# Performance work log

Measured on AMD Instinct MI355X. Metric: run time of the kernel, lower is better.

Reference implementation:

```python
import jax, jax.numpy as jnp
import numpy as np
from jax import lax

N_LAYER = 24
N_EMBD = 1024
FFN = 4 * N_EMBD
LN_EPS = 1e-5


def setup_inputs() -> dict:
    key = jax.random.key(0)
    ks = jax.random.split(key, 24)
    L, C, F = N_LAYER, N_EMBD, FFN
    s = C ** -0.5  # keep GEMV outputs O(1) so exp() stays finite

    def rn(k, shape, scale=1.0):
        return jax.random.normal(k, shape, dtype=jnp.float32) * scale

    state = jnp.concatenate([
        rn(ks[1], (1, L, C)),                                          # statea: prev ln1 output
        rn(ks[2], (1, L, C), 0.1),                                     # stateb: wkv numerator acc
        jax.random.uniform(ks[3], (1, L, C), dtype=jnp.float32) + 0.5, # statec: wkv denominator acc (>0)
        rn(ks[4], (1, L, C)),                                          # stated: prev ln2 output
    ], axis=0)

    return {
        "x": rn(ks[0], (C,)),
        "state": state,
        "ln1w": 1.0 + rn(ks[5], (L, C), 0.02),
        "ln1b": rn(ks[6], (L, C), 0.02),
        "ln2w": 1.0 + rn(ks[7], (L, C), 0.02),
        "ln2b": rn(ks[8], (L, C), 0.02),
        "time_decay": -jnp.abs(rn(ks[9], (L, C))) - 0.1,
        "time_first": rn(ks[10], (L, C), 0.1),
        "kktk": jax.random.uniform(ks[11], (L, C), dtype=jnp.float32),
        "vvtv": jax.random.uniform(ks[12], (L, C), dtype=jnp.float32),
        "rrtr": jax.random.uniform(ks[13], (L, C), dtype=jnp.float32),
        "key": rn(ks[14], (L, 3, C, C), s),        # [kk, vv, -rr] stacks
        "outputv": rn(ks[15], (L, C, C), s),
        "time_mix_k_ffn": jax.random.uniform(ks[16], (L, C), dtype=jnp.float32),
        "time_mix_r_ffn": jax.random.uniform(ks[17], (L, C), dtype=jnp.float32),
        "key_ffn": rn(ks[18], (L, F, C), s),
        "receptance_ffn": rn(ks[19], (L, C, C), s),  # stored pre-negated, as in the module
        "value_ffn": rn(ks[20], (L, C, F), F ** -0.5),
    }


def _ln(v, w, b):
    m = v.mean()
    var = ((v - m) ** 2).mean()
    return (v - m) * lax.rsqrt(var + LN_EPS) * w + b


def reference(x, state, ln1w, ln1b, ln2w, ln2b, time_decay, time_first,
              kktk, vvtv, rrtr, key, outputv, time_mix_k_ffn, time_mix_r_ffn,
              key_ffn, receptance_ffn, value_ffn):
    # offset = 0, so the state slice covers all layers
    statea, stateb, statec, stated = state[0], state[1], state[2], state[3]  # each [L, C]
    # token-shift contributions precomputed against previous-step state
    kk_s = kktk * statea
    vv_s = vvtv * statea
    rr_s = rrtr * statea
    tmk_s = time_mix_k_ffn * stated
    tmr_s = time_mix_r_ffn * stated

    def layer(xc, p):
        (l1w, l1b, l2w, l2b, td, tfst, kks, vvs, rrs, keym, outv,
         tmk, tmr, kffn, rffn, vffn, sb, sc) = p
        xy = _ln(xc, l1w, l1b)
        k = keym[0] @ (xy + kks)
        v = keym[1] @ (xy + vvs)
        r = keym[2] @ (xy + rrs)   # keym[2] holds -receptance weights
        etfk = jnp.exp(tfst + k)
        w = (sb + etfk * v) / (sc * jnp.exp(r) + jnp.exp(tfst + k + r) + sc + etfk)
        sxx = xc + outv @ w
        ek = jnp.exp(k)
        ed = jnp.exp(td)
        sb_new = sb * ed + ek * v
        sc_new = sc * ed + ek
        xx = _ln(sxx, l2w, l2b)
        kf = jnp.square(jax.nn.relu(kffn @ (xx + tmk)))
        rf = jnp.exp(rffn @ (xx + tmr))  # rffn already negated
        x_new = sxx + (vffn @ kf) / (rf + 1.0)
        return x_new, (xy, sb_new, sc_new, xx)

    xs = (ln1w, ln1b, ln2w, ln2b, time_decay, time_first, kk_s, vv_s, rr_s,
          key, outputv, tmk_s, tmr_s, key_ffn, receptance_ffn, value_ffn,
          stateb, statec)
    x_out, (sa_n, sb_n, sc_n, sd_n) = lax.scan(layer, x, xs)
    new_state = jnp.stack([sa_n, sb_n, sc_n, sd_n])  # [4, L, C]
    return x_out, new_state
```

## Files before the change

kernel.cpp:

```cpp
#include <hip/hip_runtime.h>
#include <math.h>
#include <stddef.h>

#define NLAYER 24
#define NEMBD  1024
#define NFFN   4096
#define NB     256
#define NT     256
#define LN_EPS 1e-5f

#define OUT_SA (NEMBD)
#define OUT_SB (NEMBD + NLAYER*NEMBD)
#define OUT_SC (NEMBD + 2*NLAYER*NEMBD)
#define OUT_SD (NEMBD + 3*NLAYER*NEMBD)

typedef unsigned long long u64;
typedef unsigned u32;

#define QX_OFF    0
#define QW_OFF    1024
#define QSXX_OFF  2048
#define QKFB_OFF  3072
#define QTOTAL    7168

#define LMSK  0
#define LACT  3072
#define LFF   7168
#define LLN   27648
#define LXL   27656
#define LSXL  27660
#define LRFL  27664
#define LPT   27668
#define SMTOT 27684

struct Params {
  const float *x, *state, *ln1w, *ln1b, *ln2w, *ln2b, *td, *tf, *kktk, *vvtv, *rrtr;
  const float *key, *outputv, *tmk, *tmr, *kffn, *rffn, *vffn;
  float *out;
  u64 *q;
};

__device__ __forceinline__ float wred(float v) {
#pragma unroll
  for (int o = 32; o > 0; o >>= 1) v += __shfl_xor(v, o, 64);
  return v;
}
__device__ __forceinline__ float dot4(float4 a, float4 b) {
  return a.x*b.x + a.y*b.y + a.z*b.z + a.w*b.w;
}
__device__ __forceinline__ float fcomp(float4 v, int j) {
  return j == 0 ? v.x : (j == 1 ? v.y : (j == 2 ? v.z : v.w));
}
__device__ __forceinline__ u64 qload(const u64* a) {
  return __hip_atomic_load(a, __ATOMIC_RELAXED, __HIP_MEMORY_SCOPE_AGENT);
}
__device__ __forceinline__ void qput(u64* a, float v, u32 tag) {
  u64 w = ((u64)tag << 32) | (u64)__float_as_uint(v);
  __hip_atomic_store(a, w, __ATOMIC_RELAXED, __HIP_MEMORY_SCOPE_AGENT);
}
__device__ __forceinline__ u32   qtag(u64 w) { return (u32)(w >> 32); }
__device__ __forceinline__ float qval(u64 w) { return __uint_as_float((u32)w); }

__device__ __forceinline__ void stage16(const float* g, float* l) {
  __builtin_amdgcn_global_load_lds(
      (const __attribute__((address_space(1))) unsigned int*)g,
      (__attribute__((address_space(3))) unsigned int*)l, 16, 0, 0);
}

__device__ __forceinline__ void lbar() {
  asm volatile("s_waitcnt lgkmcnt(0)" ::: "memory");
  __builtin_amdgcn_s_barrier();
  asm volatile("" ::: "memory");
}

#define POLL4(QB, IDX, TG, OUTA)                                              \
  do {                                                                        \
    u64 a0_, a1_, a2_, a3_; long cc_ = 0;                                     \
    for (;;) {                                                                \
      a0_ = qload((QB) + (IDX) + 0); a1_ = qload((QB) + (IDX) + 1);           \
      a2_ = qload((QB) + (IDX) + 2); a3_ = qload((QB) + (IDX) + 3);           \
      if (qtag(a0_) >= (TG) && qtag(a1_) >= (TG) &&                           \
          qtag(a2_) >= (TG) && qtag(a3_) >= (TG)) break;                      \
      __builtin_amdgcn_s_sleep(1);                                            \
      if (++cc_ > (1L << 20)) break;            \
    }                                                                         \
    OUTA[0] = qval(a0_); OUTA[1] = qval(a1_);                                 \
    OUTA[2] = qval(a2_); OUTA[3] = qval(a3_);                                 \
  } while (0)

__global__ void __launch_bounds__(NT, 1)
rwkv_persistent(Params p) {
  const int b    = blockIdx.x;
  const int t    = threadIdx.x;
  const int wid  = t >> 6;
  const int lane = t & 63;
  const int i0   = t * 4;
  const int myi  = b * 4 + wid;

  __shared__ float sm[SMTOT];

  u64* QX   = p.q + QX_OFF;
  u64* QW   = p.q + QW_OFF;
  u64* QSXX = p.q + QSXX_OFF;
  u64* QKFB = p.q + QKFB_OFF;

  float4 wKEY[12];
  float4 wOV[4];
  float4 wVF[16];
  float4 pA[6];
  float4 pC[5];
  float s_tf, s_sb, s_sc, s_td;

  auto loadKEY = [&](int L) {
#pragma unroll
    for (int mth = 0; mth < 3; ++mth) {
      const float* W = p.key + ((size_t)L * 3 + mth) * NEMBD * NEMBD
                     + (size_t)myi * NEMBD + lane * 4;
#pragma unroll
      for (int c = 0; c < 4; ++c)
        wKEY[mth * 4 + c] = *(const float4*)&W[c * 256];
    }
  };
  auto loadOV = [&](int L) {
    const float* W = p.outputv + ((size_t)L * NEMBD + myi) * NEMBD + lane * 4;
#pragma unroll
    for (int c = 0; c < 4; ++c)
      wOV[c] = *(const float4*)&W[c * 256];
  };
  auto loadVF = [&](int L) {
#pragma unroll
    for (int r = 0; r < 4; ++r) {
      const float* W = p.vffn + ((size_t)L * NEMBD + b * 4 + r) * NFFN + lane * 4;
#pragma unroll
      for (int c = 0; c < 4; ++c)
        wVF[r * 4 + c] = *(const float4*)&W[(wid * 4 + c) * 256];
    }
  };
  auto stageFF = [&](int L) {
    float* slab = &sm[LFF + wid * 5120];
#pragma unroll
    for (int q = 0; q < 4; ++q) {
      const float* W = p.kffn + ((size_t)L * NFFN + b * 16 + wid * 4 + q) * NEMBD;
#pragma unroll
      for (int c = 0; c < 4; ++c)
        stage16(W + c * 256 + lane * 4, slab + q * 1024 + c * 256);
    }
    const float* Wr = p.rffn + ((size_t)L * NEMBD + myi) * NEMBD;
#pragma unroll
    for (int c = 0; c < 4; ++c)
      stage16(Wr + c * 256 + lane * 4, slab + 4096 + c * 256);
  };
  auto loadPA = [&](int L) {
    const int o = L * NEMBD + i0;
    pA[0] = *(const float4*)&p.ln1w[o];
    pA[1] = *(const float4*)&p.ln1b[o];
    pA[2] = *(const float4*)&p.state[0 * NLAYER * NEMBD + o];
    pA[3] = *(const float4*)&p.kktk[o];
    pA[4] = *(const float4*)&p.vvtv[o];
    pA[5] = *(const float4*)&p.rrtr[o];
    if (lane == 0) {
      const int ix = L * NEMBD + myi;
      s_tf = p.tf[ix];
      s_sb = p.state[1 * NLAYER * NEMBD + ix];
      s_sc = p.state[2 * NLAYER * NEMBD + ix];
      s_td = p.td[ix];
    }
  };
  auto loadPC = [&](int L) {
    const int o = L * NEMBD + i0;
    pC[0] = *(const float4*)&p.ln2w[o];
    pC[1] = *(const float4*)&p.ln2b[o];
    pC[2] = *(const float4*)&p.state[3 * NLAYER * NEMBD + o];
    pC[3] = *(const float4*)&p.tmk[o];
    pC[4] = *(const float4*)&p.tmr[o];
  };

  loadPA(0); loadKEY(0); loadOV(0);

  for (int l = 0; l < NLAYER; ++l) {
    const u32 t1 = (u32)(4 * l + 1), t2 = t1 + 1, t3 = t1 + 2, t4 = t1 + 3;

    {
      float xa[4];
      if (l == 0) {
        float4 x4 = *(const float4*)&p.x[i0];
        xa[0] = x4.x; xa[1] = x4.y; xa[2] = x4.z; xa[3] = x4.w;
      } else {
        POLL4(QX, i0, (u32)(4 * l), xa);
      }
      if (t == b) {
#pragma unroll
        for (int j = 0; j < 4; ++j) sm[LXL + j] = xa[j];
      }
      float s = xa[0] + xa[1] + xa[2] + xa[3];
      float q = xa[0]*xa[0] + xa[1]*xa[1] + xa[2]*xa[2] + xa[3]*xa[3];
      s = wred(s); q = wred(q);
      if (lane == 0) { sm[LLN + wid] = s; sm[LLN + 4 + wid] = q; }
      lbar();
      float m  = (sm[LLN+0] + sm[LLN+1] + sm[LLN+2] + sm[LLN+3]) * (1.f / NEMBD);
      float tq = (sm[LLN+4] + sm[LLN+5] + sm[LLN+6] + sm[LLN+7]) * (1.f / NEMBD);
      float rs = rsqrtf(tq - m * m + LN_EPS);
#pragma unroll
      for (int j = 0; j < 4; ++j) {
        int i = i0 + j;
        float xy  = (xa[j] - m) * rs * fcomp(pA[0], j) + fcomp(pA[1], j);
        float sav = fcomp(pA[2], j);
        sm[LMSK + i]        = xy + fcomp(pA[3], j) * sav;
        sm[LMSK + 1024 + i] = xy + fcomp(pA[4], j) * sav;
        sm[LMSK + 2048 + i] = xy + fcomp(pA[5], j) * sav;
        if (t == b) p.out[OUT_SA + l * NEMBD + i] = xy;
      }
      lbar();
      float a0 = 0.f, a1 = 0.f, a2 = 0.f;
#pragma unroll
      for (int c = 0; c < 4; ++c) {
        int col = lane * 4 + c * 256;
        a0 += dot4(wKEY[c],     *(const float4*)&sm[LMSK + col]);
        a1 += dot4(wKEY[4 + c], *(const float4*)&sm[LMSK + 1024 + col]);
        a2 += dot4(wKEY[8 + c], *(const float4*)&sm[LMSK + 2048 + col]);
      }
      a0 = wred(a0); a1 = wred(a1); a2 = wred(a2);
      if (lane == 0) {
        float etfk = expf(s_tf + a0);
        float er   = expf(a2);
        float wv = (s_sb + etfk * a1) / ((s_sc + etfk) * (1.f + er));
        qput(&QW[myi], wv, t1);
        float ek = expf(a0), ed = expf(s_td);
        p.out[OUT_SB + l * NEMBD + myi] = s_sb * ed + ek * a1;
        p.out[OUT_SC + l * NEMBD + myi] = s_sc * ed + ek;
      }
      stageFF(l); loadPC(l);
      lbar();
    }

    {
      float wv[4];
      POLL4(QW, i0, t1, wv);
#pragma unroll
      for (int j = 0; j < 4; ++j) sm[LMSK + i0 + j] = wv[j];
      lbar();
      float acc = 0.f;
#pragma unroll
      for (int c = 0; c < 4; ++c)
        acc += dot4(wOV[c], *(const float4*)&sm[LMSK + lane * 4 + c * 256]);
      acc = wred(acc);
      if (lane == 0) {
        float sxx = sm[LXL + wid] + acc;
        qput(&QSXX[myi], sxx, t2);
        sm[LSXL + wid] = sxx;
      }
      loadVF(l);
      lbar();
    }

    {
      float xa[4];
      POLL4(QSXX, i0, t2, xa);
      float s = xa[0] + xa[1] + xa[2] + xa[3];
      float q = xa[0]*xa[0] + xa[1]*xa[1] + xa[2]*xa[2] + xa[3]*xa[3];
      s = wred(s); q = wred(q);
      if (lane == 0) { sm[LLN + wid] = s; sm[LLN + 4 + wid] = q; }
      lbar();
      float m  = (sm[LLN+0] + sm[LLN+1] + sm[LLN+2] + sm[LLN+3]) * (1.f / NEMBD);
      float tq = (sm[LLN+4] + sm[LLN+5] + sm[LLN+6] + sm[LLN+7]) * (1.f / NEMBD);
      float rs = rsqrtf(tq - m * m + LN_EPS);
#pragma unroll
      for (int j = 0; j < 4; ++j) {
        int i = i0 + j;
        float xx  = (xa[j] - m) * rs * fcomp(pC[0], j) + fcomp(pC[1], j);
        float sdv = fcomp(pC[2], j);
        sm[LMSK + i]        = xx + fcomp(pC[3], j) * sdv;
        sm[LMSK + 1024 + i] = xx + fcomp(pC[4], j) * sdv;
        if (t == b) p.out[OUT_SD + l * NEMBD + i] = xx;
      }
      lbar();
      const float* slab = &sm[LFF + wid * 5120];
#pragma unroll
      for (int q2 = 0; q2 < 4; ++q2) {
        float a = 0.f;
#pragma unroll
        for (int c = 0; c < 4; ++c) {
          int col = lane * 4 + c * 256;
          a += dot4(*(const float4*)&slab[q2 * 1024 + col],
                    *(const float4*)&sm[LMSK + col]);
        }
        a = wred(a);
        if (lane == 0) {
          float kv = fmaxf(a, 0.f);
          qput(&QKFB[b * 16 + wid * 4 + q2], kv * kv, t3);
        }
      }
      {
        float a = 0.f;
#pragma unroll
        for (int c = 0; c < 4; ++c) {
          int col = lane * 4 + c * 256;
          a += dot4(*(const float4*)&slab[4096 + col],
                    *(const float4*)&sm[LMSK + 1024 + col]);
        }
        a = wred(a);
        if (lane == 0) sm[LRFL + wid] = expf(a);
      }
      if (l + 1 < NLAYER) { loadKEY(l + 1); loadPA(l + 1); }
      lbar();
    }

    {
#pragma unroll
      for (int c = 0; c < 4; ++c) {
        float ka[4];
        POLL4(QKFB, c * 1024 + i0, t3, ka);
#pragma unroll
        for (int j = 0; j < 4; ++j) sm[LACT + c * 1024 + i0 + j] = ka[j];
      }
      lbar();
#pragma unroll
      for (int r = 0; r < 4; ++r) {
        float a = 0.f;
#pragma unroll
        for (int c = 0; c < 4; ++c)
          a += dot4(wVF[r * 4 + c],
                    *(const float4*)&sm[LACT + lane * 4 + (wid * 4 + c) * 256]);
        a = wred(a);
        if (lane == 0) sm[LPT + r * 4 + wid] = a;
      }
      if (l + 1 < NLAYER) loadOV(l + 1);
      lbar();
      if (t < 4) {
        float tot = sm[LPT + t * 4 + 0] + sm[LPT + t * 4 + 1]
                  + sm[LPT + t * 4 + 2] + sm[LPT + t * 4 + 3];
        float xn = sm[LSXL + t] + tot / (sm[LRFL + t] + 1.f);
        if (l == NLAYER - 1) p.out[b * 4 + t] = xn;
        else                 qput(&QX[b * 4 + t], xn, t4);
      }
    }
  }
}

__global__ void rwkv_init(u64* q) {
  for (int i = 0; i < 28; ++i)
    q[threadIdx.x * 28 + i] = 0ull;
}

extern "C" void kernel_launch(void* const* d_in, const int* in_sizes, int n_in,
                              void* d_out, int out_size, void* d_ws, size_t ws_size,
                              hipStream_t stream) {
  Params p;
  p.x       = (const float*)d_in[0];
  p.state   = (const float*)d_in[1];
  p.ln1w    = (const float*)d_in[2];
  p.ln1b    = (const float*)d_in[3];
  p.ln2w    = (const float*)d_in[4];
  p.ln2b    = (const float*)d_in[5];
  p.td      = (const float*)d_in[6];
  p.tf      = (const float*)d_in[7];
  p.kktk    = (const float*)d_in[8];
  p.vvtv    = (const float*)d_in[9];
  p.rrtr    = (const float*)d_in[10];
  p.key     = (const float*)d_in[11];
  p.outputv = (const float*)d_in[12];
  p.tmk     = (const float*)d_in[13];
  p.tmr     = (const float*)d_in[14];
  p.kffn    = (const float*)d_in[15];
  p.rffn    = (const float*)d_in[16];
  p.vffn    = (const float*)d_in[17];
  p.out     = (float*)d_out;
  p.q       = (u64*)d_ws;

  rwkv_init<<<1, NB, 0, stream>>>(p.q);
  rwkv_persistent<<<NB, NT, 0, stream>>>(p);
}
```

Measured before the change: 450.5 us.

## Specialize one wave as cross-block poller and split GEMV work across three waves

Wave 3 of each block becomes a dedicated communication wave that polls the global tagged queues with coalesced per-lane loads and signals the three compute waves through an LDS generation counter. The compute waves split the key/value/receptance rows by matrix instead of by row, redistribute the FFN rows and value-FFN columns across three waves, and stage per-layer LN and mix parameters into LDS asynchronously instead of holding them in registers. The aim is to cut polling overhead and barrier stalls and to overlap weight prefetch with communication. In exchange, compute parallelism drops from four waves to three, and the spin handshake on a volatile LDS word adds latency and fragility.

```diff
diff --git a/kernel.cpp b/kernel.cpp
--- a/kernel.cpp
+++ b/kernel.cpp
@@ -23,15 +23,17 @@
 #define QKFB_OFF  3072
 #define QTOTAL    7168
 
-#define LMSK  0
-#define LACT  3072
-#define LFF   7168
-#define LLN   27648
-#define LXL   27656
-#define LSXL  27660
-#define LRFL  27664
-#define LPT   27668
-#define SMTOT 27684
+#define LACT  0
+#define LMSK  4096
+#define LPRM  7168
+#define LFF   13312
+#define LKVR  34816
+#define LLN   34828
+#define LXL   34836
+#define LSXL  34840
+#define LRFL  34844
+#define LPT   34848
+#define SMTOT 34860
 
 struct Params {
   const float *x, *state, *ln1w, *ln1b, *ln2w, *ln2b, *td, *tf, *kktk, *vvtv, *rrtr;
@@ -48,9 +50,6 @@
 __device__ __forceinline__ float dot4(float4 a, float4 b) {
   return a.x*b.x + a.y*b.y + a.z*b.z + a.w*b.w;
 }
-__device__ __forceinline__ float fcomp(float4 v, int j) {
-  return j == 0 ? v.x : (j == 1 ? v.y : (j == 2 ? v.z : v.w));
-}
 __device__ __forceinline__ u64 qload(const u64* a) {
   return __hip_atomic_load(a, __ATOMIC_RELAXED, __HIP_MEMORY_SCOPE_AGENT);
 }
@@ -73,19 +72,21 @@
   asm volatile("" ::: "memory");
 }
 
-#define POLL4(QB, IDX, TG, OUTA)                                              \
+#define POLLS(N, QB, TG, LOFF)                                                \
   do {                                                                        \
-    u64 a0_, a1_, a2_, a3_; long cc_ = 0;                                     \
+    u64 pw_[N]; long cc_ = 0;                                                 \
     for (;;) {                                                                \
-      a0_ = qload((QB) + (IDX) + 0); a1_ = qload((QB) + (IDX) + 1);           \
-      a2_ = qload((QB) + (IDX) + 2); a3_ = qload((QB) + (IDX) + 3);           \
-      if (qtag(a0_) >= (TG) && qtag(a1_) >= (TG) &&                           \
-          qtag(a2_) >= (TG) && qtag(a3_) >= (TG)) break;                      \
+      bool ok_ = true;                                                        \
+      _Pragma("unroll")                                                       \
+      for (int c_ = 0; c_ < N; ++c_) pw_[c_] = qload((QB) + c_*64 + lane);    \
+      _Pragma("unroll")                                                       \
+      for (int c_ = 0; c_ < N; ++c_) ok_ &= (qtag(pw_[c_]) >= (TG));          \
+      if (__all(ok_)) break;                                                  \
       __builtin_amdgcn_s_sleep(1);                                            \
       if (++cc_ > (1L << 20)) break;            \
     }                                                                         \
-    OUTA[0] = qval(a0_); OUTA[1] = qval(a1_);                                 \
-    OUTA[2] = qval(a2_); OUTA[3] = qval(a3_);                                 \
+    _Pragma("unroll")                                                         \
+    for (int c_ = 0; c_ < N; ++c_) sm[(LOFF) + c_*64 + lane] = qval(pw_[c_]); \
   } while (0)
 
 __global__ void __launch_bounds__(NT, 1)
@@ -95,103 +96,125 @@
   const int wid  = t >> 6;
   const int lane = t & 63;
   const int i0   = t * 4;
-  const int myi  = b * 4 + wid;
+  const bool w3  = (wid == 3);
+  const int cw   = wid;
 
   __shared__ float sm[SMTOT];
+  __shared__ unsigned genw_s;
+  volatile unsigned* gw = &genw_s;
+
+  if (t == 0) genw_s = 0u;
+  __syncthreads();
 
   u64* QX   = p.q + QX_OFF;
   u64* QW   = p.q + QW_OFF;
   u64* QSXX = p.q + QSXX_OFF;
   u64* QKFB = p.q + QKFB_OFF;
 
-  float4 wKEY[12];
+  float4 wKEY[16];
   float4 wOV[4];
-  float4 wVF[16];
-  float4 pA[6];
-  float4 pC[5];
+  float4 wVF[24];
   float s_tf, s_sb, s_sc, s_td;
 
   auto loadKEY = [&](int L) {
-#pragma unroll
-    for (int mth = 0; mth < 3; ++mth) {
-      const float* W = p.key + ((size_t)L * 3 + mth) * NEMBD * NEMBD
-                     + (size_t)myi * NEMBD + lane * 4;
+    const float* W = p.key + ((size_t)L * 3 + cw) * NEMBD * NEMBD
+                   + (size_t)(b * 4) * NEMBD + lane * 4;
+#pragma unroll
+    for (int idx = 0; idx < 4; ++idx)
 #pragma unroll
       for (int c = 0; c < 4; ++c)
-        wKEY[mth * 4 + c] = *(const float4*)&W[c * 256];
-    }
-  };
-  auto loadOV = [&](int L) {
-    const float* W = p.outputv + ((size_t)L * NEMBD + myi) * NEMBD + lane * 4;
+        wKEY[idx * 4 + c] = *(const float4*)&W[(size_t)idx * NEMBD + c * 256];
+  };
+  auto loadOV = [&](int L, int row) {
+    const float* W = p.outputv + ((size_t)L * NEMBD + b * 4 + row) * NEMBD + lane * 4;
 #pragma unroll
     for (int c = 0; c < 4; ++c)
       wOV[c] = *(const float4*)&W[c * 256];
   };
   auto loadVF = [&](int L) {
+    const int jb = (cw == 0) ? 0 : ((cw == 1) ? 6 : 11);
+    const int jn = (cw == 0) ? 6 : 5;
 #pragma unroll
     for (int r = 0; r < 4; ++r) {
       const float* W = p.vffn + ((size_t)L * NEMBD + b * 4 + r) * NFFN + lane * 4;
 #pragma unroll
-      for (int c = 0; c < 4; ++c)
-        wVF[r * 4 + c] = *(const float4*)&W[(wid * 4 + c) * 256];
+      for (int c = 0; c < 6; ++c) if (c < jn)
+        wVF[r * 6 + c] = *(const float4*)&W[(jb + c) * 256];
     }
   };
   auto stageFF = [&](int L) {
-    float* slab = &sm[LFF + wid * 5120];
-#pragma unroll
-    for (int q = 0; q < 4; ++q) {
-      const float* W = p.kffn + ((size_t)L * NFFN + b * 16 + wid * 4 + q) * NEMBD;
-#pragma unroll
-      for (int c = 0; c < 4; ++c)
-        stage16(W + c * 256 + lane * 4, slab + q * 1024 + c * 256);
-    }
-    const float* Wr = p.rffn + ((size_t)L * NEMBD + myi) * NEMBD;
+    float* slab = &sm[LFF + cw * 7168];
+#pragma unroll
+    for (int e = 0; e < 7; ++e) {
+      const int f = cw * 7 + e;
+      if (f < 20) {
+        const float* W = (f < 16)
+          ? p.kffn + ((size_t)L * NFFN  + b * 16 + f) * NEMBD
+          : p.rffn + ((size_t)L * NEMBD + b * 4 + (f - 16)) * NEMBD;
+#pragma unroll
+        for (int c = 0; c < 4; ++c)
+          stage16(W + c * 256 + lane * 4, slab + e * 1024 + c * 256);
+      }
+    }
+  };
+  auto stagePrm = [&](const float* src, int L, int v) {
 #pragma unroll
     for (int c = 0; c < 4; ++c)
-      stage16(Wr + c * 256 + lane * 4, slab + 4096 + c * 256);
-  };
-  auto loadPA = [&](int L) {
-    const int o = L * NEMBD + i0;
-    pA[0] = *(const float4*)&p.ln1w[o];
-    pA[1] = *(const float4*)&p.ln1b[o];
-    pA[2] = *(const float4*)&p.state[0 * NLAYER * NEMBD + o];
-    pA[3] = *(const float4*)&p.kktk[o];
-    pA[4] = *(const float4*)&p.vvtv[o];
-    pA[5] = *(const float4*)&p.rrtr[o];
-    if (lane == 0) {
-      const int ix = L * NEMBD + myi;
-      s_tf = p.tf[ix];
-      s_sb = p.state[1 * NLAYER * NEMBD + ix];
-      s_sc = p.state[2 * NLAYER * NEMBD + ix];
-      s_td = p.td[ix];
-    }
-  };
-  auto loadPC = [&](int L) {
-    const int o = L * NEMBD + i0;
-    pC[0] = *(const float4*)&p.ln2w[o];
-    pC[1] = *(const float4*)&p.ln2b[o];
-    pC[2] = *(const float4*)&p.state[3 * NLAYER * NEMBD + o];
-    pC[3] = *(const float4*)&p.tmk[o];
-    pC[4] = *(const float4*)&p.tmr[o];
-  };
-
-  loadPA(0); loadKEY(0); loadOV(0);
+      stage16(src + L * NEMBD + c * 256 + lane * 4, &sm[LPRM + v * 1024 + c * 256]);
+  };
+  auto stagePA = [&](int L) {
+    if (cw == 0) { stagePrm(p.ln1w, L, 0); stagePrm(p.ln1b, L, 1); }
+    if (cw == 1) { stagePrm(p.state + 0 * NLAYER * NEMBD, L, 2); stagePrm(p.kktk, L, 3); }
+    if (cw == 2) { stagePrm(p.vvtv, L, 4); stagePrm(p.rrtr, L, 5); }
+  };
+  auto stagePC = [&](int L) {
+    if (cw == 0) { stagePrm(p.ln2w, L, 0); stagePrm(p.ln2b, L, 1); }
+    if (cw == 1) { stagePrm(p.state + 3 * NLAYER * NEMBD, L, 2); stagePrm(p.tmk, L, 3); }
+    if (cw == 2) { stagePrm(p.tmr, L, 4); }
+  };
+  auto spin = [&](unsigned v) {
+    long c = 0;
+    while (*gw < v) { __builtin_amdgcn_s_sleep(1); if (++c > (1L << 20)) break; }
+    asm volatile("" ::: "memory");
+    asm volatile("s_waitcnt vmcnt(0)" ::: "memory");
+  };
+  auto post = [&](unsigned v) {
+    asm volatile("s_waitcnt lgkmcnt(0)" ::: "memory");
+    if (lane == 0) *gw = v;
+  };
+
+  if (!w3) { loadKEY(0); loadOV(0, cw); stagePA(0); }
 
   for (int l = 0; l < NLAYER; ++l) {
     const u32 t1 = (u32)(4 * l + 1), t2 = t1 + 1, t3 = t1 + 2, t4 = t1 + 3;
-
+    const u32 g1 = (u32)(4 * l + 1), g2 = g1 + 1, g3 = g1 + 2, g4 = g1 + 3;
+
+    if (w3) {
+      if (l == 0) {
+#pragma unroll
+        for (int c = 0; c < 4; ++c) {
+          float4 xv = *(const float4*)&p.x[c * 256 + lane * 4];
+          *(float4*)&sm[LACT + c * 256 + lane * 4] = xv;
+        }
+      } else {
+        POLLS(16, QX, (u32)(4 * l), LACT);
+      }
+      if (lane < 4) {
+        const int ix = l * NEMBD + b * 4 + lane;
+        s_tf = p.tf[ix];
+        s_sb = p.state[1 * NLAYER * NEMBD + ix];
+        s_sc = p.state[2 * NLAYER * NEMBD + ix];
+        s_td = p.td[ix];
+      }
+      loadOV(l, 3);
+      post(g1);
+    } else {
+      spin(g1);
+    }
     {
       float xa[4];
-      if (l == 0) {
-        float4 x4 = *(const float4*)&p.x[i0];
-        xa[0] = x4.x; xa[1] = x4.y; xa[2] = x4.z; xa[3] = x4.w;
-      } else {
-        POLL4(QX, i0, (u32)(4 * l), xa);
-      }
-      if (t == b) {
-#pragma unroll
-        for (int j = 0; j < 4; ++j) sm[LXL + j] = xa[j];
-      }
+#pragma unroll
+      for (int j = 0; j < 4; ++j) xa[j] = sm[LACT + i0 + j];
       float s = xa[0] + xa[1] + xa[2] + xa[3];
       float q = xa[0]*xa[0] + xa[1]*xa[1] + xa[2]*xa[2] + xa[3]*xa[3];
       s = wred(s); q = wred(q);
@@ -203,59 +226,81 @@
 #pragma unroll
       for (int j = 0; j < 4; ++j) {
         int i = i0 + j;
-        float xy  = (xa[j] - m) * rs * fcomp(pA[0], j) + fcomp(pA[1], j);
-        float sav = fcomp(pA[2], j);
-        sm[LMSK + i]        = xy + fcomp(pA[3], j) * sav;
-        sm[LMSK + 1024 + i] = xy + fcomp(pA[4], j) * sav;
-        sm[LMSK + 2048 + i] = xy + fcomp(pA[5], j) * sav;
+        float xy  = (xa[j] - m) * rs * sm[LPRM + i] + sm[LPRM + 1024 + i];
+        float sav = sm[LPRM + 2048 + i];
+        sm[LMSK + i]        = xy + sm[LPRM + 3072 + i] * sav;
+        sm[LMSK + 1024 + i] = xy + sm[LPRM + 4096 + i] * sav;
+        sm[LMSK + 2048 + i] = xy + sm[LPRM + 5120 + i] * sav;
         if (t == b) p.out[OUT_SA + l * NEMBD + i] = xy;
       }
+      if (t == b) {
+#pragma unroll
+        for (int j = 0; j < 4; ++j) sm[LXL + j] = xa[j];
+      }
       lbar();
-      float a0 = 0.f, a1 = 0.f, a2 = 0.f;
-#pragma unroll
-      for (int c = 0; c < 4; ++c) {
-        int col = lane * 4 + c * 256;
-        a0 += dot4(wKEY[c],     *(const float4*)&sm[LMSK + col]);
-        a1 += dot4(wKEY[4 + c], *(const float4*)&sm[LMSK + 1024 + col]);
-        a2 += dot4(wKEY[8 + c], *(const float4*)&sm[LMSK + 2048 + col]);
-      }
-      a0 = wred(a0); a1 = wred(a1); a2 = wred(a2);
+      if (!w3) {
+        const float* mv = &sm[LMSK + cw * 1024];
+#pragma unroll
+        for (int idx = 0; idx < 4; ++idx) {
+          float a = 0.f;
+#pragma unroll
+          for (int c = 0; c < 4; ++c)
+            a += dot4(wKEY[idx * 4 + c], *(const float4*)&mv[lane * 4 + c * 256]);
+          a = wred(a);
+          if (lane == 0) sm[LKVR + cw * 4 + idx] = a;
+        }
+      }
+      lbar();
+      if (w3 && lane < 4) {
+        float k = sm[LKVR + lane], v = sm[LKVR + 4 + lane], r = sm[LKVR + 8 + lane];
+        float etfk = expf(s_tf + k);
+        float er   = expf(r);
+        float wv = (s_sb + etfk * v) / ((s_sc + etfk) * (1.f + er));
+        qput(&QW[b * 4 + lane], wv, t1);
+        float ek = expf(k), ed = expf(s_td);
+        p.out[OUT_SB + l * NEMBD + b * 4 + lane] = s_sb * ed + ek * v;
+        p.out[OUT_SC + l * NEMBD + b * 4 + lane] = s_sc * ed + ek;
+      }
+    }
+
+    if (w3) {
+      POLLS(16, QW, t1, LMSK);
+      post(g2);
+      float a = 0.f;
+#pragma unroll
+      for (int c = 0; c < 4; ++c)
+        a += dot4(wOV[c], *(const float4*)&sm[LMSK + lane * 4 + c * 256]);
+      a = wred(a);
       if (lane == 0) {
-        float etfk = expf(s_tf + a0);
-        float er   = expf(a2);
-        float wv = (s_sb + etfk * a1) / ((s_sc + etfk) * (1.f + er));
-        qput(&QW[myi], wv, t1);
-        float ek = expf(a0), ed = expf(s_td);
-        p.out[OUT_SB + l * NEMBD + myi] = s_sb * ed + ek * a1;
-        p.out[OUT_SC + l * NEMBD + myi] = s_sc * ed + ek;
-      }
-      stageFF(l); loadPC(l);
-      lbar();
-    }
-
-    {
-      float wv[4];
-      POLL4(QW, i0, t1, wv);
-#pragma unroll
-      for (int j = 0; j < 4; ++j) sm[LMSK + i0 + j] = wv[j];
-      lbar();
-      float acc = 0.f;
+        float sxx = sm[LXL + 3] + a;
+        qput(&QSXX[b * 4 + 3], sxx, t2);
+        sm[LSXL + 3] = sxx;
+      }
+    } else {
+      spin(g2);
+      float a = 0.f;
 #pragma unroll
       for (int c = 0; c < 4; ++c)
-        acc += dot4(wOV[c], *(const float4*)&sm[LMSK + lane * 4 + c * 256]);
-      acc = wred(acc);
+        a += dot4(wOV[c], *(const float4*)&sm[LMSK + lane * 4 + c * 256]);
+      a = wred(a);
       if (lane == 0) {
-        float sxx = sm[LXL + wid] + acc;
-        qput(&QSXX[myi], sxx, t2);
-        sm[LSXL + wid] = sxx;
-      }
-      loadVF(l);
-      lbar();
-    }
-
+        float sxx = sm[LXL + cw] + a;
+        qput(&QSXX[b * 4 + cw], sxx, t2);
+        sm[LSXL + cw] = sxx;
+      }
+      stageFF(l); stagePC(l);
+    }
+
+    if (w3) {
+      POLLS(16, QSXX, t2, LACT);
+      post(g3);
+    } else {
+      spin(g3);
+    }
     {
       float xa[4];
-      POLL4(QSXX, i0, t2, xa);
+#pragma unroll
+      for (int j = 0; j < 4; ++j) xa[j] = sm[LACT + i0 + j];
       float s = xa[0] + xa[1] + xa[2] + xa[3];
       float q = xa[0]*xa[0] + xa[1]*xa[1] + xa[2]*xa[2] + xa[3]*xa[3];
       s = wred(s); q = wred(q);
@@ -267,72 +312,64 @@
 #pragma unroll
       for (int j = 0; j < 4; ++j) {
         int i = i0 + j;
-        float xx  = (xa[j] - m) * rs * fcomp(pC[0], j) + fcomp(pC[1], j);
-        float sdv = fcomp(pC[2], j);
-        sm[LMSK + i]        = xx + fcomp(pC[3], j) * sdv;
-        sm[LMSK + 1024 + i] = xx + fcomp(pC[4], j) * sdv;
+        float xx  = (xa[j] - m) * rs * sm[LPRM + i] + sm[LPRM + 1024 + i];
+        float sdv = sm[LPRM + 2048 + i];
+        sm[LMSK + i]        = xx + sm[LPRM + 3072 + i] * sdv;
+        sm[LMSK + 1024 + i] = xx + sm[LPRM + 4096 + i] * sdv;
         if (t == b) p.out[OUT_SD + l * NEMBD + i] = xx;
       }
       lbar();
-      const float* slab = &sm[LFF + wid * 5120];
-#pragma unroll
-      for (int q2 = 0; q2 < 4; ++q2) {
-        float a = 0.f;
-#pragma unroll
-        for (int c = 0; c < 4; ++c) {
-          int col = lane * 4 + c * 256;
-          a += dot4(*(const float4*)&slab[q2 * 1024 + col],
-                    *(const float4*)&sm[LMSK + col]);
+      if (!w3) {
+        const float* slab = &sm[LFF + cw * 7168];
+#pragma unroll
+        for (int e = 0; e < 7; ++e) {
+          const int f = cw * 7 + e;
+          if (f < 20) {
+            const float* mv = &sm[LMSK + ((f < 16) ? 0 : 1024)];
+            float a = 0.f;
+#pragma unroll
+            for (int c = 0; c < 4; ++c) {
+              int col = lane * 4 + c * 256;
+              a += dot4(*(const float4*)&slab[e * 1024 + col],
+                        *(const float4*)&mv[col]);
+            }
+            a = wred(a);
+            if (lane == 0) {
+              if (f < 16) { float kv = fmaxf(a, 0.f); qput(&QKFB[b * 16 + f], kv * kv, t3); }
+              else        { sm[LRFL + (f - 16)] = expf(a); }
+            }
+          }
         }
-        a = wred(a);
-        if (lane == 0) {
-          float kv = fmaxf(a, 0.f);
-          qput(&QKFB[b * 16 + wid * 4 + q2], kv * kv, t3);
-        }
-      }
-      {
-        float a = 0.f;
-#pragma unroll
-        for (int c = 0; c < 4; ++c) {
-          int col = lane * 4 + c * 256;
-          a += dot4(*(const float4*)&slab[4096 + col],
-                    *(const float4*)&sm[LMSK + 1024 + col]);
-        }
-        a = wred(a);
-        if (lane == 0) sm[LRFL + wid] = expf(a);
-      }
-      if (l + 1 < NLAYER) { loadKEY(l + 1); loadPA(l + 1); }
-      lbar();
-    }
-
-    {
-#pragma unroll
-      for (int c = 0; c < 4; ++c) {
-        float ka[4];
-        POLL4(QKFB, c * 1024 + i0, t3, ka);
-#pragma unroll
-        for (int j = 0; j < 4; ++j) sm[LACT + c * 1024 + i0 + j] = ka[j];
-      }
-      lbar();
+        loadVF(l);
+      }
+    }
+
+    if (w3) {
+      POLLS(32, QKFB, t3, LACT);
+      POLLS(32, QKFB + 2048, t3, LACT + 2048);
+      post(g4);
+    } else {
+      spin(g4);
+      const int jb = (cw == 0) ? 0 : ((cw == 1) ? 6 : 11);
+      const int jn = (cw == 0) ? 6 : 5;
 #pragma unroll
       for (int r = 0; r < 4; ++r) {
         float a = 0.f;
 #pragma unroll
-        for (int c = 0; c < 4; ++c)
-          a += dot4(wVF[r * 4 + c],
-                    *(const float4*)&sm[LACT + lane * 4 + (wid * 4 + c) * 256]);
+        for (int c = 0; c < 6; ++c) if (c < jn)
+          a += dot4(wVF[r * 6 + c],
+                    *(const float4*)&sm[LACT + lane * 4 + (jb + c) * 256]);
         a = wred(a);
-        if (lane == 0) sm[LPT + r * 4 + wid] = a;
-      }
-      if (l + 1 < NLAYER) loadOV(l + 1);
-      lbar();
-      if (t < 4) {
-        float tot = sm[LPT + t * 4 + 0] + sm[LPT + t * 4 + 1]
-                  + sm[LPT + t * 4 + 2] + sm[LPT + t * 4 + 3];
-        float xn = sm[LSXL + t] + tot / (sm[LRFL + t] + 1.f);
-        if (l == NLAYER - 1) p.out[b * 4 + t] = xn;
-        else                 qput(&QX[b * 4 + t], xn, t4);
-      }
+        if (lane == 0) sm[LPT + r * 3 + cw] = a;
+      }
+      if (l + 1 < NLAYER) { loadKEY(l + 1); loadOV(l + 1, cw); stagePA(l + 1); }
+    }
+    lbar();
+    if (w3 && lane < 4) {
+      float tot = sm[LPT + lane * 3] + sm[LPT + lane * 3 + 1] + sm[LPT + lane * 3 + 2];
+      float xn  = sm[LSXL + lane] + tot / (sm[LRFL + lane] + 1.f);
+      if (l == NLAYER - 1) p.out[b * 4 + lane] = xn;
+      else                 qput(&QX[b * 4 + lane], xn, t4);
     }
   }
 }
```

After: 611.1 us. 35.7% more time.

## Double persistent grid to 512 blocks with two output rows per block

Applied to the files above, without the earlier changes.

Doubles the persistent grid from 256 to 512 blocks so each block owns two output rows instead of four. Per-block weight registers and shared-memory slabs are halved, and launch bounds now allow two blocks per CU. The key GEMV is split across warps by matrix (k, v, r), which adds an extra barrier and a shared-memory handoff. The aim is more memory-level parallelism across CUs for the bandwidth-bound GEMVs, at the cost of more blocks taking part in the flag-polling global syncs and some warps sitting idle in several phases.

```diff
diff --git a/kernel.cpp b/kernel.cpp
--- a/kernel.cpp
+++ b/kernel.cpp
@@ -5,7 +5,7 @@
 #define NLAYER 24
 #define NEMBD  1024
 #define NFFN   4096
-#define NB     256
+#define NB     512
 #define NT     256
 #define LN_EPS 1e-5f
 
@@ -23,15 +23,17 @@
 #define QKFB_OFF  3072
 #define QTOTAL    7168
 
-#define LMSK  0
-#define LACT  3072
-#define LFF   7168
-#define LLN   27648
-#define LXL   27656
-#define LSXL  27660
-#define LRFL  27664
-#define LPT   27668
-#define SMTOT 27684
+#define LFF   0
+#define LACT  10240
+#define LMSK  11264
+#define LKF   10240
+#define LLN   15360
+#define LKVR  15368
+#define LXL   15376
+#define LSXL  15378
+#define LRFL  15380
+#define LPT   15382
+#define SMTOT 15390
 
 struct Params {
   const float *x, *state, *ln1w, *ln1b, *ln2w, *ln2b, *td, *tf, *kktk, *vvtv, *rrtr;
@@ -88,14 +90,13 @@
     OUTA[2] = qval(a2_); OUTA[3] = qval(a3_);                                 \
   } while (0)
 
-__global__ void __launch_bounds__(NT, 1)
+__global__ void __launch_bounds__(NT, 2)
 rwkv_persistent(Params p) {
   const int b    = blockIdx.x;
   const int t    = threadIdx.x;
   const int wid  = t >> 6;
   const int lane = t & 63;
   const int i0   = t * 4;
-  const int myi  = b * 4 + wid;
 
   __shared__ float sm[SMTOT];
 
@@ -104,51 +105,57 @@
   u64* QSXX = p.q + QSXX_OFF;
   u64* QKFB = p.q + QKFB_OFF;
 
-  float4 wKEY[12];
+  float4 wKEY[8];
   float4 wOV[4];
-  float4 wVF[16];
+  float4 wVF[8];
   float4 pA[6];
   float4 pC[5];
   float s_tf, s_sb, s_sc, s_td;
 
   auto loadKEY = [&](int L) {
-#pragma unroll
-    for (int mth = 0; mth < 3; ++mth) {
-      const float* W = p.key + ((size_t)L * 3 + mth) * NEMBD * NEMBD
-                     + (size_t)myi * NEMBD + lane * 4;
+    if (wid < 3) {
+      const float* W = p.key + ((size_t)L * 3 + wid) * NEMBD * NEMBD
+                     + (size_t)(b * 2) * NEMBD + lane * 4;
+#pragma unroll
+      for (int idx = 0; idx < 2; ++idx)
+#pragma unroll
+        for (int c = 0; c < 4; ++c)
+          wKEY[idx * 4 + c] = *(const float4*)&W[(size_t)idx * NEMBD + c * 256];
+    }
+  };
+  auto loadOV = [&](int L) {
+    if (wid < 2) {
+      const float* W = p.outputv + ((size_t)L * NEMBD + b * 2 + wid) * NEMBD + lane * 4;
 #pragma unroll
       for (int c = 0; c < 4; ++c)
-        wKEY[mth * 4 + c] = *(const float4*)&W[c * 256];
-    }
-  };
-  auto loadOV = [&](int L) {
-    const float* W = p.outputv + ((size_t)L * NEMBD + myi) * NEMBD + lane * 4;
-#pragma unroll
-    for (int c = 0; c < 4; ++c)
-      wOV[c] = *(const float4*)&W[c * 256];
+        wOV[c] = *(const float4*)&W[c * 256];
+    }
   };
   auto loadVF = [&](int L) {
 #pragma unroll
-    for (int r = 0; r < 4; ++r) {
-      const float* W = p.vffn + ((size_t)L * NEMBD + b * 4 + r) * NFFN + lane * 4;
+    for (int r = 0; r < 2; ++r) {
+      const float* W = p.vffn + ((size_t)L * NEMBD + b * 2 + r) * NFFN
+                     + wid * 1024 + lane * 4;
 #pragma unroll
       for (int c = 0; c < 4; ++c)
-        wVF[r * 4 + c] = *(const float4*)&W[(wid * 4 + c) * 256];
+        wVF[r * 4 + c] = *(const float4*)&W[c * 256];
     }
   };
   auto stageFF = [&](int L) {
-    float* slab = &sm[LFF + wid * 5120];
-#pragma unroll
-    for (int q = 0; q < 4; ++q) {
-      const float* W = p.kffn + ((size_t)L * NFFN + b * 16 + wid * 4 + q) * NEMBD;
-#pragma unroll
-      for (int c = 0; c < 4; ++c)
-        stage16(W + c * 256 + lane * 4, slab + q * 1024 + c * 256);
-    }
-    const float* Wr = p.rffn + ((size_t)L * NEMBD + myi) * NEMBD;
-#pragma unroll
-    for (int c = 0; c < 4; ++c)
-      stage16(Wr + c * 256 + lane * 4, slab + 4096 + c * 256);
+#pragma unroll
+    for (int e = 0; e < 2; ++e) {
+      const int f = wid * 2 + e;
+      const float* W = p.kffn + ((size_t)L * NFFN + b * 8 + f) * NEMBD + lane * 4;
+      float* dst = &sm[LFF + f * 1024];
+#pragma unroll
+      for (int c = 0; c < 4; ++c) stage16(W + c * 256, dst + c * 256);
+    }
+    if (wid < 2) {
+      const float* Wr = p.rffn + ((size_t)L * NEMBD + b * 2 + wid) * NEMBD + lane * 4;
+      float* dr = &sm[LFF + (8 + wid) * 1024];
+#pragma unroll
+      for (int c = 0; c < 4; ++c) stage16(Wr + c * 256, dr + c * 256);
+    }
   };
   auto loadPA = [&](int L) {
     const int o = L * NEMBD + i0;
@@ -158,13 +165,6 @@
     pA[3] = *(const float4*)&p.kktk[o];
     pA[4] = *(const float4*)&p.vvtv[o];
     pA[5] = *(const float4*)&p.rrtr[o];
-    if (lane == 0) {
-      const int ix = L * NEMBD + myi;
-      s_tf = p.tf[ix];
-      s_sb = p.state[1 * NLAYER * NEMBD + ix];
-      s_sc = p.state[2 * NLAYER * NEMBD + ix];
-      s_td = p.td[ix];
-    }
   };
   auto loadPC = [&](int L) {
     const int o = L * NEMBD + i0;
@@ -174,11 +174,21 @@
     pC[3] = *(const float4*)&p.tmk[o];
     pC[4] = *(const float4*)&p.tmr[o];
   };
-
-  loadPA(0); loadKEY(0); loadOV(0);
+  auto loadSC = [&](int L) {
+    if (wid == 3 && lane < 2) {
+      const int ix = L * NEMBD + b * 2 + lane;
+      s_tf = p.tf[ix];
+      s_sb = p.state[1 * NLAYER * NEMBD + ix];
+      s_sc = p.state[2 * NLAYER * NEMBD + ix];
+      s_td = p.td[ix];
+    }
+  };
+
+  loadPA(0); loadKEY(0); loadOV(0); loadSC(0);
 
   for (int l = 0; l < NLAYER; ++l) {
     const u32 t1 = (u32)(4 * l + 1), t2 = t1 + 1, t3 = t1 + 2, t4 = t1 + 3;
+    const bool last = (l == NLAYER - 1);
 
     {
       float xa[4];
@@ -188,9 +198,10 @@
       } else {
         POLL4(QX, i0, (u32)(4 * l), xa);
       }
-      if (t == b) {
-#pragma unroll
-        for (int j = 0; j < 4; ++j) sm[LXL + j] = xa[j];
+#pragma unroll
+      for (int r = 0; r < 2; ++r) {
+        int gi = b * 2 + r;
+        if (t == (gi >> 2)) sm[LXL + r] = xa[gi & 3];
       }
       float s = xa[0] + xa[1] + xa[2] + xa[3];
       float q = xa[0]*xa[0] + xa[1]*xa[1] + xa[2]*xa[2] + xa[3]*xa[3];
@@ -208,46 +219,52 @@
         sm[LMSK + i]        = xy + fcomp(pA[3], j) * sav;
         sm[LMSK + 1024 + i] = xy + fcomp(pA[4], j) * sav;
         sm[LMSK + 2048 + i] = xy + fcomp(pA[5], j) * sav;
-        if (t == b) p.out[OUT_SA + l * NEMBD + i] = xy;
-      }
-      lbar();
-      float a0 = 0.f, a1 = 0.f, a2 = 0.f;
-#pragma unroll
-      for (int c = 0; c < 4; ++c) {
-        int col = lane * 4 + c * 256;
-        a0 += dot4(wKEY[c],     *(const float4*)&sm[LMSK + col]);
-        a1 += dot4(wKEY[4 + c], *(const float4*)&sm[LMSK + 1024 + col]);
-        a2 += dot4(wKEY[8 + c], *(const float4*)&sm[LMSK + 2048 + col]);
-      }
-      a0 = wred(a0); a1 = wred(a1); a2 = wred(a2);
-      if (lane == 0) {
-        float etfk = expf(s_tf + a0);
-        float er   = expf(a2);
-        float wv = (s_sb + etfk * a1) / ((s_sc + etfk) * (1.f + er));
-        qput(&QW[myi], wv, t1);
-        float ek = expf(a0), ed = expf(s_td);
-        p.out[OUT_SB + l * NEMBD + myi] = s_sb * ed + ek * a1;
-        p.out[OUT_SC + l * NEMBD + myi] = s_sc * ed + ek;
+        if (t == (b & 255)) p.out[OUT_SA + l * NEMBD + i] = xy;
+      }
+      lbar();
+      if (wid < 3) {
+        const float* mv = &sm[LMSK + wid * 1024];
+#pragma unroll
+        for (int idx = 0; idx < 2; ++idx) {
+          float a = 0.f;
+#pragma unroll
+          for (int c = 0; c < 4; ++c)
+            a += dot4(wKEY[idx * 4 + c], *(const float4*)&mv[lane * 4 + c * 256]);
+          a = wred(a);
+          if (lane == 0) sm[LKVR + wid * 2 + idx] = a;
+        }
+      }
+      lbar();
+      if (wid == 3 && lane < 2) {
+        float k = sm[LKVR + lane], v = sm[LKVR + 2 + lane], r = sm[LKVR + 4 + lane];
+        float etfk = expf(s_tf + k);
+        float er   = expf(r);
+        float wv = (s_sb + etfk * v) / ((s_sc + etfk) * (1.f + er));
+        qput(&QW[b * 2 + lane], wv, t1);
+        float ek = expf(k), ed = expf(s_td);
+        p.out[OUT_SB + l * NEMBD + b * 2 + lane] = s_sb * ed + ek * v;
+        p.out[OUT_SC + l * NEMBD + b * 2 + lane] = s_sc * ed + ek;
       }
       stageFF(l); loadPC(l);
-      lbar();
     }
 
     {
       float wv[4];
       POLL4(QW, i0, t1, wv);
 #pragma unroll
-      for (int j = 0; j < 4; ++j) sm[LMSK + i0 + j] = wv[j];
-      lbar();
-      float acc = 0.f;
-#pragma unroll
-      for (int c = 0; c < 4; ++c)
-        acc += dot4(wOV[c], *(const float4*)&sm[LMSK + lane * 4 + c * 256]);
-      acc = wred(acc);
-      if (lane == 0) {
-        float sxx = sm[LXL + wid] + acc;
-        qput(&QSXX[myi], sxx, t2);
-        sm[LSXL + wid] = sxx;
+      for (int j = 0; j < 4; ++j) sm[LACT + i0 + j] = wv[j];
+      lbar();
+      if (wid < 2) {
+        float a = 0.f;
+#pragma unroll
+        for (int c = 0; c < 4; ++c)
+          a += dot4(wOV[c], *(const float4*)&sm[LACT + lane * 4 + c * 256]);
+        a = wred(a);
+        if (lane == 0) {
+          float sxx = sm[LXL + wid] + a;
+          qput(&QSXX[b * 2 + wid], sxx, t2);
+          sm[LSXL + wid] = sxx;
+        }
       }
       loadVF(l);
       lbar();
@@ -271,37 +288,41 @@
         float sdv = fcomp(pC[2], j);
         sm[LMSK + i]        = xx + fcomp(pC[3], j) * sdv;
         sm[LMSK + 1024 + i] = xx + fcomp(pC[4], j) * sdv;
-        if (t == b) p.out[OUT_SD + l * NEMBD + i] = xx;
-      }
-      lbar();
-      const float* slab = &sm[LFF + wid * 5120];
-#pragma unroll
-      for (int q2 = 0; q2 < 4; ++q2) {
-        float a = 0.f;
-#pragma unroll
-        for (int c = 0; c < 4; ++c) {
-          int col = lane * 4 + c * 256;
-          a += dot4(*(const float4*)&slab[q2 * 1024 + col],
-                    *(const float4*)&sm[LMSK + col]);
+        if (t == (b & 255)) p.out[OUT_SD + l * NEMBD + i] = xx;
+      }
+      lbar();
+      {
+        const float* mk = &sm[LMSK];
+#pragma unroll
+        for (int e = 0; e < 2; ++e) {
+          const int f = wid * 2 + e;
+          const float* slab = &sm[LFF + f * 1024];
+          float a = 0.f;
+#pragma unroll
+          for (int c = 0; c < 4; ++c) {
+            int col = lane * 4 + c * 256;
+            a += dot4(*(const float4*)&slab[col], *(const float4*)&mk[col]);
+          }
+          a = wred(a);
+          if (lane == 0) {
+            float kv = fmaxf(a, 0.f);
+            qput(&QKFB[b * 8 + f], kv * kv, t3);
+          }
         }
-        a = wred(a);
-        if (lane == 0) {
-          float kv = fmaxf(a, 0.f);
-          qput(&QKFB[b * 16 + wid * 4 + q2], kv * kv, t3);
+        if (wid < 2) {
+          const float* slab = &sm[LFF + (8 + wid) * 1024];
+          const float* mr = &sm[LMSK + 1024];
+          float a = 0.f;
+#pragma unroll
+          for (int c = 0; c < 4; ++c) {
+            int col = lane * 4 + c * 256;
+            a += dot4(*(const float4*)&slab[col], *(const float4*)&mr[col]);
+          }
+          a = wred(a);
+          if (lane == 0) sm[LRFL + wid] = expf(a);
         }
       }
-      {
-        float a = 0.f;
-#pragma unroll
-        for (int c = 0; c < 4; ++c) {
-          int col = lane * 4 + c * 256;
-          a += dot4(*(const float4*)&slab[4096 + col],
-                    *(const float4*)&sm[LMSK + 1024 + col]);
-        }
-        a = wred(a);
-        if (lane == 0) sm[LRFL + wid] = expf(a);
-      }
-      if (l + 1 < NLAYER) { loadKEY(l + 1); loadPA(l + 1); }
+      if (!last) { loadKEY(l + 1); loadPA(l + 1); loadSC(l + 1); }
       lbar();
     }
 
@@ -311,27 +332,27 @@
         float ka[4];
         POLL4(QKFB, c * 1024 + i0, t3, ka);
 #pragma unroll
-        for (int j = 0; j < 4; ++j) sm[LACT + c * 1024 + i0 + j] = ka[j];
-      }
-      lbar();
-#pragma unroll
-      for (int r = 0; r < 4; ++r) {
+        for (int j = 0; j < 4; ++j) sm[LKF + c * 1024 + i0 + j] = ka[j];
+      }
+      lbar();
+#pragma unroll
+      for (int r = 0; r < 2; ++r) {
+        const float* kf = &sm[LKF + wid * 1024];
         float a = 0.f;
 #pragma unroll
         for (int c = 0; c < 4; ++c)
-          a += dot4(wVF[r * 4 + c],
-                    *(const float4*)&sm[LACT + lane * 4 + (wid * 4 + c) * 256]);
+          a += dot4(wVF[r * 4 + c], *(const float4*)&kf[lane * 4 + c * 256]);
         a = wred(a);
         if (lane == 0) sm[LPT + r * 4 + wid] = a;
       }
-      if (l + 1 < NLAYER) loadOV(l + 1);
-      lbar();
-      if (t < 4) {
+      if (!last) loadOV(l + 1);
+      lbar();
+      if (t < 2) {
         float tot = sm[LPT + t * 4 + 0] + sm[LPT + t * 4 + 1]
                   + sm[LPT + t * 4 + 2] + sm[LPT + t * 4 + 3];
         float xn = sm[LSXL + t] + tot / (sm[LRFL + t] + 1.f);
-        if (l == NLAYER - 1) p.out[b * 4 + t] = xn;
-        else                 qput(&QX[b * 4 + t], xn, t4);
+        if (last) p.out[b * 2 + t] = xn;
+        else      qput(&QX[b * 2 + t], xn, t4);
       }
     }
   }
@@ -367,6 +388,6 @@
   p.out     = (float*)d_out;
   p.q       = (u64*)d_ws;
 
-  rwkv_init<<<1, NB, 0, stream>>>(p.q);
+  rwkv_init<<<1, NT, 0, stream>>>(p.q);
   rwkv_persistent<<<NB, NT, 0, stream>>>(p);
 }
```

After: 650.8 us. 44.5% more time.
